# Kernel optimization log

Measured on AMD Instinct MI355X. Metric: run time of the kernel, lower is better.

## Reference

```python
import jax, jax.numpy as jnp
import numpy as np

N = 50000      # nodes
E = 800000     # edges
D = 128        # in_dim == hidden_dim
L = 5          # num GIN layers
G = 1000       # graphs in batch


def setup_inputs() -> dict:
    key = jax.random.key(0)
    ks = jax.random.split(key, 6)
    s = 1.0 / np.sqrt(D)  # keep activations stable over 5 layers
    x = jax.random.normal(ks[0], (N, D), dtype=jnp.float32)
    edge_index = jax.random.randint(ks[1], (2, E), 0, N, dtype=jnp.int32)
    batch = jnp.sort(jax.random.randint(ks[2], (N,), 0, G, dtype=jnp.int32))
    W1s = jax.random.normal(ks[3], (L, D, D), dtype=jnp.float32) * s
    b1s = jnp.zeros((L, D), jnp.float32)
    W2s = jax.random.normal(ks[4], (L, D, D), dtype=jnp.float32) * s
    b2s = jnp.zeros((L, D), jnp.float32)
    Wh = jax.random.normal(ks[5], (D, 1), dtype=jnp.float32) * s
    bh = jnp.zeros((1,), jnp.float32)
    return {"x": x, "edge_index": edge_index, "batch": batch,
            "W1s": W1s, "b1s": b1s, "W2s": W2s, "b2s": b2s,
            "Wh": Wh, "bh": bh}


def reference(x, edge_index, batch, W1s, b1s, W2s, b2s, Wh, bh):
    src, dst = edge_index[0], edge_index[1]
    h = x
    for l in range(L):
        # GINConv with eps=0: mlp(x + sum_{j->i} x_j)
        aggr = jax.ops.segment_sum(h[src], dst, num_segments=N)  # [N, D]
        z = h + aggr
        z = jax.nn.relu(z @ W1s[l] + b1s[l]) @ W2s[l] + b2s[l]   # 2-layer MLP
        h = jax.nn.relu(z)  # outer F.relu; dropout is identity in eval
    # global mean pool per graph
    sums = jax.ops.segment_sum(h, batch, num_segments=G)                     # [G, D]
    cnts = jax.ops.segment_sum(jnp.ones((N, 1), h.dtype), batch, num_segments=G)
    pooled = sums / jnp.maximum(cnts, 1.0)
    return pooled @ Wh + bh  # [G, 1] logits
```

## Files before the change

kernel.cpp:

```cpp
#include <hip/hip_runtime.h>
#include <hip/hip_bf16.h>

#define D 128
#define SLOTS 64
#define CSTR 72
#define BCAP 9216

typedef short short8 __attribute__((ext_vector_type(8)));
typedef float f32x4 __attribute__((ext_vector_type(4)));
typedef unsigned short u16;
typedef unsigned int u32;

static __device__ __forceinline__ u16 f2bf(float f) {
  union { float f; unsigned u; } v; v.f = f;
  unsigned r = v.u + 0x7FFF + ((v.u >> 16) & 1);
  return (u16)(r >> 16);
}
static __device__ __forceinline__ float bf2f(u16 h) {
  union { unsigned u; float f; } v; v.u = ((unsigned)h) << 16;
  return v.f;
}

__global__ __launch_bounds__(1024) void prep_kernel(
    const int* __restrict__ src, const int* __restrict__ dst,
    const float* __restrict__ x, const float* __restrict__ W1,
    const float* __restrict__ W2, int* __restrict__ gcount,
    u32* __restrict__ bedge, u16* __restrict__ W1th, u16* __restrict__ W1tl,
    u16* __restrict__ W2th, u16* __restrict__ W2tl, u32* __restrict__ xp,
    u32* __restrict__ hp, int E, int nbk, int wtotal, int nPairs,
    int nA, int nB, int nC, int N, int rowsP) {
  __shared__ int cnt[128];
  __shared__ int base[128];
  int b = blockIdx.x, t = threadIdx.x;
  if (b < nA) {
    if (t < nbk) cnt[t] = 0;
    __syncthreads();
    int e = b * 1024 + t;
    int bk = 0, p = 0;
    u32 payload = 0;
    bool valid = e < E;
    if (valid) {
      int d = dst[e];
      bk = d >> 9;
      payload = ((u32)src[e] << 9) | (u32)(d & 511);
      p = atomicAdd(&cnt[bk], 1);
    }
    __syncthreads();
    if (t < nbk) base[t] = cnt[t] ? atomicAdd(&gcount[t], cnt[t]) : 0;
    __syncthreads();
    if (valid) {
      int pos = base[bk] + p;
      if (pos < BCAP) bedge[(size_t)bk * BCAP + pos] = payload;
    }
  } else if (b < nA + nB) {
    int idx = (b - nA) * 1024 + t;
    if (idx < wtotal) {
      int l = idx >> 14;
      int r = idx & 16383;
      int j = r & 7;
      int lane = (r >> 3) & 63;
      int tt = r >> 9;
      int kt = tt >> 3, nt = tt & 7;
      int k = kt * 32 + (lane >> 4) * 8 + j;
      int n = nt * 16 + (lane & 15);
      size_t s = (size_t)l * D * D + (size_t)k * D + n;
      float w1 = W1[s], w2 = W2[s];
      u16 h1 = f2bf(w1), h2 = f2bf(w2);
      W1th[idx] = h1; W1tl[idx] = f2bf(w1 - bf2f(h1));
      W2th[idx] = h2; W2tl[idx] = f2bf(w2 - bf2f(h2));
    }
  } else if (b < nA + nB + nC) {
    int i0 = (b - nA - nB) * 4096 + t * 4;
    if (i0 < nPairs) {
      int node = i0 >> 6, pr = i0 & 63;
      float4 f0 = ((const float4*)x)[i0 >> 1];
      float4 f1 = ((const float4*)x)[(i0 >> 1) + 1];
      uint4 o;
      o.x = ((u32)f2bf(f0.y) << 16) | f2bf(f0.x);
      o.y = ((u32)f2bf(f0.w) << 16) | f2bf(f0.z);
      o.z = ((u32)f2bf(f1.y) << 16) | f2bf(f1.x);
      o.w = ((u32)f2bf(f1.w) << 16) | f2bf(f1.z);
      *(uint4*)(xp + ((size_t)(pr >> 5) * rowsP + node) * 32 + (pr & 31)) = o;
    }
  } else {
    if (t < 64) {
      xp[((size_t)(t >> 5) * rowsP + N) * 32 + (t & 31)] = 0;
      hp[((size_t)(t >> 5) * rowsP + N) * 32 + (t & 31)] = 0;
    }
  }
}

__global__ __launch_bounds__(1024) void binB_kernel(
    const int* __restrict__ gcount, const u32* __restrict__ bedge,
    int* __restrict__ deg, u16* __restrict__ colidx, int N) {
  __shared__ int cnt2[512];
  int b = blockIdx.x;
  int t = threadIdx.x;
  if (t < 512) cnt2[t] = 0;
  __syncthreads();
  int count = min(gcount[b], BCAP);
  const u32* lst = bedge + (size_t)b * BCAP;
  for (int i = t; i < count; i += 1024) {
    u32 v = lst[i];
    int local = v & 511;
    int slot = atomicAdd(&cnt2[local], 1);
    if (slot < SLOTS)
      colidx[((size_t)(b << 9) + local) * CSTR + slot] = (u16)(v >> 9);
  }
  __syncthreads();
  if (t < 512) {
    int node = (b << 9) + t;
    if (node < N) deg[node] = min(cnt2[t], SLOTS);
  }
  for (int i = t; i < 512 * CSTR; i += 1024) {
    int local = i / CSTR;
    int slot = i - local * CSTR;
    int node = (b << 9) + local;
    if (node < N && slot >= min(cnt2[local], SLOTS))
      colidx[((size_t)(b << 9) + local) * CSTR + slot] = (u16)N;
  }
}

__global__ __launch_bounds__(256) void aggregate_kernel(
    const u32* __restrict__ hp, const int* __restrict__ deg,
    const u16* __restrict__ colidx, u32* __restrict__ zp, int N, int rowsP) {
  int p = blockIdx.x & 1;
  int chunk = blockIdx.x >> 1;
  int lane = threadIdx.x & 63;
  int wave = threadIdx.x >> 6;
  int g = lane >> 3, c = lane & 7;
  int node = chunk * 32 + wave * 8 + g;
  bool live = node < N;
  const uint4* hpp = (const uint4*)(hp + (size_t)p * rowsP * 32);
  int e = live ? deg[node] : 0;
  int em = max(e, __shfl_xor(e, 8, 64));
  em = max(em, __shfl_xor(em, 16, 64));
  em = max(em, __shfl_xor(em, 32, 64));
  const u16* nbr = colidx + (size_t)(live ? node : 0) * CSTR;
  uint4 s = hpp[(size_t)(live ? node : N) * 8 + c];
  float a0 = bf2f((u16)(s.x & 0xffff)), a1 = bf2f((u16)(s.x >> 16));
  float a2 = bf2f((u16)(s.y & 0xffff)), a3 = bf2f((u16)(s.y >> 16));
  float a4 = bf2f((u16)(s.z & 0xffff)), a5 = bf2f((u16)(s.z >> 16));
  float a6 = bf2f((u16)(s.w & 0xffff)), a7 = bf2f((u16)(s.w >> 16));
  for (int k = 0; k < em; k += 8) {
    int idx[8];
    uint4 v[8];
#pragma unroll
    for (int i = 0; i < 8; ++i) idx[i] = nbr[k + i];
#pragma unroll
    for (int i = 0; i < 8; ++i) v[i] = hpp[(size_t)idx[i] * 8 + c];
#pragma unroll
    for (int i = 0; i < 8; ++i) {
      a0 += bf2f((u16)(v[i].x & 0xffff)); a1 += bf2f((u16)(v[i].x >> 16));
      a2 += bf2f((u16)(v[i].y & 0xffff)); a3 += bf2f((u16)(v[i].y >> 16));
      a4 += bf2f((u16)(v[i].z & 0xffff)); a5 += bf2f((u16)(v[i].z >> 16));
      a6 += bf2f((u16)(v[i].w & 0xffff)); a7 += bf2f((u16)(v[i].w >> 16));
    }
  }
  if (live) {
    uint4 o;
    o.x = ((u32)f2bf(a1) << 16) | f2bf(a0);
    o.y = ((u32)f2bf(a3) << 16) | f2bf(a2);
    o.z = ((u32)f2bf(a5) << 16) | f2bf(a4);
    o.w = ((u32)f2bf(a7) << 16) | f2bf(a6);
    ((uint4*)(zp + (size_t)p * rowsP * 32))[(size_t)node * 8 + c] = o;
  }
}

template <int STAGE>
__global__ __launch_bounds__(256) void gemm_kernel(
    const u16* __restrict__ A, const u16* __restrict__ Wth, const u16* __restrict__ Wtl,
    const float* __restrict__ bias, u16* __restrict__ outp,
    const float* __restrict__ Wh, const int* __restrict__ batch, float* __restrict__ gsum,
    int nrows, int rowsP) {
  __shared__ __attribute__((aligned(16))) u16 ldsW[32768];
  u16* ldsWh = ldsW;
  u16* ldsWl = ldsW + 16384;
  int tid = threadIdx.x;
  {
    const uint4* gh = (const uint4*)Wth;
    const uint4* gl = (const uint4*)Wtl;
    uint4 th[8], tl[8];
#pragma unroll
    for (int i = 0; i < 8; ++i) { th[i] = gh[tid + i * 256]; tl[i] = gl[tid + i * 256]; }
    uint4* lh = (uint4*)ldsWh;
    uint4* ll = (uint4*)ldsWl;
#pragma unroll
    for (int i = 0; i < 8; ++i) { lh[tid + i * 256] = th[i]; ll[tid + i * 256] = tl[i]; }
  }
  int wave = tid >> 6, lane = tid & 63;
  int quad = lane >> 4, l16 = lane & 15;
  int rowbase = blockIdx.x * 128 + wave * 32;
  int mc0 = min(rowbase + l16, nrows - 1);
  int mc1 = min(rowbase + 16 + l16, nrows - 1);

  short8 a0[4], a1[4];
#pragma unroll
  for (int kt = 0; kt < 4; ++kt) {
    if (STAGE == 0) {
      const u16* base = A + ((size_t)(kt >> 1) * rowsP) * 64 + (kt & 1) * 32 + quad * 8;
      a0[kt] = *(const short8*)(base + (size_t)mc0 * 64);
      a1[kt] = *(const short8*)(base + (size_t)mc1 * 64);
    } else {
      a0[kt] = *(const short8*)(A + (size_t)mc0 * D + kt * 32 + quad * 8);
      a1[kt] = *(const short8*)(A + (size_t)mc1 * D + kt * 32 + quad * 8);
    }
  }

  __syncthreads();

  f32x4 acc[2][8];
  f32x4 zero = {0.f, 0.f, 0.f, 0.f};
#pragma unroll
  for (int mt = 0; mt < 2; ++mt)
#pragma unroll
    for (int nt = 0; nt < 8; ++nt) acc[mt][nt] = zero;

#pragma unroll
  for (int kt = 0; kt < 4; ++kt) {
#pragma unroll
    for (int nt = 0; nt < 8; ++nt) {
      int fo = ((kt * 8 + nt) * 64 + lane) * 8;
      short8 bh = *(const short8*)(ldsWh + fo);
      short8 bl = *(const short8*)(ldsWl + fo);
      acc[0][nt] = __builtin_amdgcn_mfma_f32_16x16x32_bf16(a0[kt], bh, acc[0][nt], 0, 0, 0);
      acc[0][nt] = __builtin_amdgcn_mfma_f32_16x16x32_bf16(a0[kt], bl, acc[0][nt], 0, 0, 0);
      acc[1][nt] = __builtin_amdgcn_mfma_f32_16x16x32_bf16(a1[kt], bh, acc[1][nt], 0, 0, 0);
      acc[1][nt] = __builtin_amdgcn_mfma_f32_16x16x32_bf16(a1[kt], bl, acc[1][nt], 0, 0, 0);
    }
  }

  if (STAGE == 2) {
    float dotr[2][4] = {{0.f, 0.f, 0.f, 0.f}, {0.f, 0.f, 0.f, 0.f}};
#pragma unroll
    for (int nt = 0; nt < 8; ++nt) {
      int col = nt * 16 + l16;
      float bv = bias[col];
      float wv = Wh[col];
#pragma unroll
      for (int mt = 0; mt < 2; ++mt)
#pragma unroll
        for (int r = 0; r < 4; ++r)
          dotr[mt][r] += fmaxf(acc[mt][nt][r] + bv, 0.f) * wv;
    }
#pragma unroll
    for (int m = 1; m < 16; m <<= 1) {
#pragma unroll
      for (int mt = 0; mt < 2; ++mt)
#pragma unroll
        for (int r = 0; r < 4; ++r) dotr[mt][r] += __shfl_xor(dotr[mt][r], m, 64);
    }
    if (l16 == 0) {
#pragma unroll
      for (int mt = 0; mt < 2; ++mt)
#pragma unroll
        for (int r = 0; r < 4; ++r) {
          int row = rowbase + mt * 16 + quad * 4 + r;
          if (row < nrows) atomicAdd(&gsum[batch[row]], dotr[mt][r]);
        }
    }
  } else {
    __syncthreads();
#pragma unroll
    for (int nt = 0; nt < 8; ++nt) {
      float bv = bias[nt * 16 + l16];
#pragma unroll
      for (int mt = 0; mt < 2; ++mt)
#pragma unroll
        for (int r = 0; r < 4; ++r) {
          int lrow = wave * 32 + mt * 16 + quad * 4 + r;
          ldsW[lrow * 136 + nt * 16 + l16] = f2bf(fmaxf(acc[mt][nt][r] + bv, 0.f));
        }
    }
    __syncthreads();
#pragma unroll
    for (int i = 0; i < 8; ++i) {
      int chunk = i * 256 + tid;
      int r = chunk >> 4;
      int cc = (chunk & 15) * 8;
      int row = blockIdx.x * 128 + r;
      if (row < nrows) {
        uint4 v = *(const uint4*)(ldsW + r * 136 + cc);
        if (STAGE == 0) {
          *(uint4*)(outp + (size_t)row * D + cc) = v;
        } else {
          *(uint4*)(outp + ((size_t)(cc >> 6) * rowsP + row) * 64 + (cc & 63)) = v;
        }
      }
    }
  }
}

__global__ void pool_final_kernel(const float* __restrict__ gsum, const int* __restrict__ batch,
                                  const float* __restrict__ bh, float* __restrict__ out,
                                  int G, int N) {
  int g = blockIdx.x * 256 + threadIdx.x;
  if (g >= G) return;
  int lo = 0, hi = N;
  while (lo < hi) { int mid = (lo + hi) >> 1; if (batch[mid] < g) lo = mid + 1; else hi = mid; }
  int lo2 = lo, hi2 = N;
  while (lo2 < hi2) { int mid = (lo2 + hi2) >> 1; if (batch[mid] < g + 1) lo2 = mid + 1; else hi2 = mid; }
  int c = lo2 - lo;
  out[g] = gsum[g] / fmaxf((float)c, 1.f) + bh[0];
}

extern "C" void kernel_launch(void* const* d_in, const int* in_sizes, int n_in,
                              void* d_out, int out_size, void* d_ws, size_t ws_size,
                              hipStream_t stream) {
  const float* x   = (const float*)d_in[0];
  const int* eidx  = (const int*)d_in[1];
  const int* batch = (const int*)d_in[2];
  const float* W1s = (const float*)d_in[3];
  const float* b1s = (const float*)d_in[4];
  const float* W2s = (const float*)d_in[5];
  const float* b2s = (const float*)d_in[6];
  const float* Wh  = (const float*)d_in[7];
  const float* bh  = (const float*)d_in[8];
  float* out = (float*)d_out;

  int N = in_sizes[0] / D;
  int E = in_sizes[1] / 2;
  int G = out_size;
  int L = in_sizes[3] / (D * D);
  int nbk = (N + 511) >> 9;
  int wtotal = L * D * D;
  int nPairs = N * D / 2;
  int rowsP = N + 1;

  const int* src = eidx;
  const int* dst = eidx + E;

  char* p = (char*)d_ws;
  auto alloc = [&](size_t b) { char* r = p; p += (b + 255) & ~(size_t)255; return r; };
  u16*   hpnl   = (u16*)  alloc((size_t)2 * rowsP * 64 * 2);
  u16*   xpnl   = (u16*)  alloc((size_t)2 * rowsP * 64 * 2);
  u16*   zpnl   = (u16*)  alloc((size_t)2 * rowsP * 64 * 2);
  u16*   yb     = (u16*)  alloc((size_t)N * D * 2);
  size_t zbytes = (size_t)G * 4 + 512;
  char*  zblk   =         alloc(zbytes);
  float* gsum   = (float*)zblk;
  int*   gcount = (int*)(zblk + (size_t)G * 4);
  int*   deg    = (int*)  alloc((size_t)N * 4);
  u16*   colidx = (u16*)  alloc((size_t)N * CSTR * 2);
  u32*   bedge  = (u32*)  alloc((size_t)128 * BCAP * 4);
  u16*   W1th   = (u16*)  alloc((size_t)L * D * D * 2);
  u16*   W1tl   = (u16*)  alloc((size_t)L * D * D * 2);
  u16*   W2th   = (u16*)  alloc((size_t)L * D * D * 2);
  u16*   W2tl   = (u16*)  alloc((size_t)L * D * D * 2);

  hipMemsetAsync(zblk, 0, zbytes, stream);

  int nA = (E + 1023) / 1024;
  int nB = (wtotal + 1023) / 1024;
  int nC = (nPairs / 4 + 1023) / 1024;
  prep_kernel<<<nA + nB + nC + 1, 1024, 0, stream>>>(
      src, dst, x, W1s, W2s, gcount, bedge, W1th, W1tl, W2th, W2tl,
      (u32*)xpnl, (u32*)hpnl, E, nbk, wtotal, nPairs, nA, nB, nC, N, rowsP);
  binB_kernel<<<nbk, 1024, 0, stream>>>(gcount, bedge, deg, colidx, N);

  int agg_blocks = 2 * ((N + 31) / 32);
  int gemm_blocks = (N + 127) / 128;
  for (int l = 0; l < L; ++l) {
    const u16* hin = (l == 0) ? xpnl : hpnl;
    size_t wo = (size_t)l * D * D;
    aggregate_kernel<<<agg_blocks, 256, 0, stream>>>(
        (const u32*)hin, deg, colidx, (u32*)zpnl, N, rowsP);
    gemm_kernel<0><<<gemm_blocks, 256, 0, stream>>>(
        zpnl, W1th + wo, W1tl + wo, b1s + (size_t)l * D, yb,
        nullptr, nullptr, nullptr, N, rowsP);
    if (l < L - 1) {
      gemm_kernel<1><<<gemm_blocks, 256, 0, stream>>>(
          yb, W2th + wo, W2tl + wo, b2s + (size_t)l * D, hpnl,
          nullptr, nullptr, nullptr, N, rowsP);
    } else {
      gemm_kernel<2><<<gemm_blocks, 256, 0, stream>>>(
          yb, W2th + wo, W2tl + wo, b2s + (size_t)l * D, nullptr,
          Wh, batch, gsum, N, rowsP);
    }
  }
  pool_final_kernel<<<(G + 255) / 256, 256, 0, stream>>>(gsum, batch, bh, out, G, N);
}
```

Baseline: 391.0 us.

## Fuse the two MLP GEMMs into one kernel keeping hidden activations in LDS

Merges the first and second MLP GEMM kernels into one per-layer mlp_kernel. The intermediate relu(zW1+b1) tile is written to shared memory and reloaded as MFMA A-fragments instead of round-tripping through a global bf16 buffer. Both weight matrices are prefetched into registers up front, with W2 swapped into LDS between the two GEMMs. This removes one launch per layer and the global write and read of the hidden tensor, at the cost of higher register pressure (four 8-element uint4 weight arrays held at once) and extra block barriers.

```diff
diff --git a/kernel.cpp b/kernel.cpp
--- a/kernel.cpp
+++ b/kernel.cpp
@@ -167,44 +167,48 @@
   }
 }
 
-template <int STAGE>
-__global__ __launch_bounds__(256) void gemm_kernel(
-    const u16* __restrict__ A, const u16* __restrict__ Wth, const u16* __restrict__ Wtl,
-    const float* __restrict__ bias, u16* __restrict__ outp,
-    const float* __restrict__ Wh, const int* __restrict__ batch, float* __restrict__ gsum,
+template <int LAST>
+__global__ __launch_bounds__(256) void mlp_kernel(
+    const u16* __restrict__ A,
+    const u16* __restrict__ W1th, const u16* __restrict__ W1tl, const float* __restrict__ b1,
+    const u16* __restrict__ W2th, const u16* __restrict__ W2tl, const float* __restrict__ b2,
+    u16* __restrict__ hout, const float* __restrict__ Wh,
+    const int* __restrict__ batch, float* __restrict__ gsum,
     int nrows, int rowsP) {
   __shared__ __attribute__((aligned(16))) u16 ldsW[32768];
   u16* ldsWh = ldsW;
   u16* ldsWl = ldsW + 16384;
   int tid = threadIdx.x;
-  {
-    const uint4* gh = (const uint4*)Wth;
-    const uint4* gl = (const uint4*)Wtl;
-    uint4 th[8], tl[8];
-#pragma unroll
-    for (int i = 0; i < 8; ++i) { th[i] = gh[tid + i * 256]; tl[i] = gl[tid + i * 256]; }
-    uint4* lh = (uint4*)ldsWh;
-    uint4* ll = (uint4*)ldsWl;
-#pragma unroll
-    for (int i = 0; i < 8; ++i) { lh[tid + i * 256] = th[i]; ll[tid + i * 256] = tl[i]; }
-  }
   int wave = tid >> 6, lane = tid & 63;
   int quad = lane >> 4, l16 = lane & 15;
   int rowbase = blockIdx.x * 128 + wave * 32;
   int mc0 = min(rowbase + l16, nrows - 1);
   int mc1 = min(rowbase + 16 + l16, nrows - 1);
 
+  uint4 t1h[8], t1l[8], t2h[8], t2l[8];
+  {
+    const uint4* g1h = (const uint4*)W1th;
+    const uint4* g1l = (const uint4*)W1tl;
+    const uint4* g2h = (const uint4*)W2th;
+    const uint4* g2l = (const uint4*)W2tl;
+#pragma unroll
+    for (int i = 0; i < 8; ++i) {
+      t1h[i] = g1h[tid + i * 256]; t1l[i] = g1l[tid + i * 256];
+      t2h[i] = g2h[tid + i * 256]; t2l[i] = g2l[tid + i * 256];
+    }
+  }
   short8 a0[4], a1[4];
 #pragma unroll
   for (int kt = 0; kt < 4; ++kt) {
-    if (STAGE == 0) {
-      const u16* base = A + ((size_t)(kt >> 1) * rowsP) * 64 + (kt & 1) * 32 + quad * 8;
-      a0[kt] = *(const short8*)(base + (size_t)mc0 * 64);
-      a1[kt] = *(const short8*)(base + (size_t)mc1 * 64);
-    } else {
-      a0[kt] = *(const short8*)(A + (size_t)mc0 * D + kt * 32 + quad * 8);
-      a1[kt] = *(const short8*)(A + (size_t)mc1 * D + kt * 32 + quad * 8);
-    }
+    const u16* base = A + ((size_t)(kt >> 1) * rowsP) * 64 + (kt & 1) * 32 + quad * 8;
+    a0[kt] = *(const short8*)(base + (size_t)mc0 * 64);
+    a1[kt] = *(const short8*)(base + (size_t)mc1 * 64);
+  }
+  {
+    uint4* lh = (uint4*)ldsWh;
+    uint4* ll = (uint4*)ldsWl;
+#pragma unroll
+    for (int i = 0; i < 8; ++i) { lh[tid + i * 256] = t1h[i]; ll[tid + i * 256] = t1l[i]; }
   }
 
   __syncthreads();
@@ -215,7 +219,6 @@
   for (int mt = 0; mt < 2; ++mt)
 #pragma unroll
     for (int nt = 0; nt < 8; ++nt) acc[mt][nt] = zero;
-
 #pragma unroll
   for (int kt = 0; kt < 4; ++kt) {
 #pragma unroll
@@ -230,12 +233,62 @@
     }
   }
 
-  if (STAGE == 2) {
+  __syncthreads();
+
+  u16* yw = ldsW + wave * 32 * 136;
+#pragma unroll
+  for (int nt = 0; nt < 8; ++nt) {
+    float bv = b1[nt * 16 + l16];
+#pragma unroll
+    for (int mt = 0; mt < 2; ++mt)
+#pragma unroll
+      for (int r = 0; r < 4; ++r) {
+        int lrow = mt * 16 + quad * 4 + r;
+        yw[lrow * 136 + nt * 16 + l16] = f2bf(fmaxf(acc[mt][nt][r] + bv, 0.f));
+      }
+  }
+  short8 p0[4], p1[4];
+#pragma unroll
+  for (int kt = 0; kt < 4; ++kt) {
+    p0[kt] = *(const short8*)(yw + (size_t)l16 * 136 + kt * 32 + quad * 8);
+    p1[kt] = *(const short8*)(yw + (size_t)(16 + l16) * 136 + kt * 32 + quad * 8);
+  }
+
+  __syncthreads();
+
+  {
+    uint4* lh = (uint4*)ldsWh;
+    uint4* ll = (uint4*)ldsWl;
+#pragma unroll
+    for (int i = 0; i < 8; ++i) { lh[tid + i * 256] = t2h[i]; ll[tid + i * 256] = t2l[i]; }
+  }
+
+  __syncthreads();
+
+#pragma unroll
+  for (int mt = 0; mt < 2; ++mt)
+#pragma unroll
+    for (int nt = 0; nt < 8; ++nt) acc[mt][nt] = zero;
+#pragma unroll
+  for (int kt = 0; kt < 4; ++kt) {
+#pragma unroll
+    for (int nt = 0; nt < 8; ++nt) {
+      int fo = ((kt * 8 + nt) * 64 + lane) * 8;
+      short8 bh = *(const short8*)(ldsWh + fo);
+      short8 bl = *(const short8*)(ldsWl + fo);
+      acc[0][nt] = __builtin_amdgcn_mfma_f32_16x16x32_bf16(p0[kt], bh, acc[0][nt], 0, 0, 0);
+      acc[0][nt] = __builtin_amdgcn_mfma_f32_16x16x32_bf16(p0[kt], bl, acc[0][nt], 0, 0, 0);
+      acc[1][nt] = __builtin_amdgcn_mfma_f32_16x16x32_bf16(p1[kt], bh, acc[1][nt], 0, 0, 0);
+      acc[1][nt] = __builtin_amdgcn_mfma_f32_16x16x32_bf16(p1[kt], bl, acc[1][nt], 0, 0, 0);
+    }
+  }
+
+  if (LAST) {
     float dotr[2][4] = {{0.f, 0.f, 0.f, 0.f}, {0.f, 0.f, 0.f, 0.f}};
 #pragma unroll
     for (int nt = 0; nt < 8; ++nt) {
       int col = nt * 16 + l16;
-      float bv = bias[col];
+      float bv = b2[col];
       float wv = Wh[col];
 #pragma unroll
       for (int mt = 0; mt < 2; ++mt)
@@ -263,7 +316,7 @@
     __syncthreads();
 #pragma unroll
     for (int nt = 0; nt < 8; ++nt) {
-      float bv = bias[nt * 16 + l16];
+      float bv = b2[nt * 16 + l16];
 #pragma unroll
       for (int mt = 0; mt < 2; ++mt)
 #pragma unroll
@@ -281,11 +334,7 @@
       int row = blockIdx.x * 128 + r;
       if (row < nrows) {
         uint4 v = *(const uint4*)(ldsW + r * 136 + cc);
-        if (STAGE == 0) {
-          *(uint4*)(outp + (size_t)row * D + cc) = v;
-        } else {
-          *(uint4*)(outp + ((size_t)(cc >> 6) * rowsP + row) * 64 + (cc & 63)) = v;
-        }
+        *(uint4*)(hout + ((size_t)(cc >> 6) * rowsP + row) * 64 + (cc & 63)) = v;
       }
     }
   }
@@ -335,7 +384,6 @@
   u16*   hpnl   = (u16*)  alloc((size_t)2 * rowsP * 64 * 2);
   u16*   xpnl   = (u16*)  alloc((size_t)2 * rowsP * 64 * 2);
   u16*   zpnl   = (u16*)  alloc((size_t)2 * rowsP * 64 * 2);
-  u16*   yb     = (u16*)  alloc((size_t)N * D * 2);
   size_t zbytes = (size_t)G * 4 + 512;
   char*  zblk   =         alloc(zbytes);
   float* gsum   = (float*)zblk;
@@ -359,23 +407,22 @@
   binB_kernel<<<nbk, 1024, 0, stream>>>(gcount, bedge, deg, colidx, N);
 
   int agg_blocks = 2 * ((N + 31) / 32);
-  int gemm_blocks = (N + 127) / 128;
+  int mlp_blocks = (N + 127) / 128;
   for (int l = 0; l < L; ++l) {
     const u16* hin = (l == 0) ? xpnl : hpnl;
     size_t wo = (size_t)l * D * D;
     aggregate_kernel<<<agg_blocks, 256, 0, stream>>>(
         (const u32*)hin, deg, colidx, (u32*)zpnl, N, rowsP);
-    gemm_kernel<0><<<gemm_blocks, 256, 0, stream>>>(
-        zpnl, W1th + wo, W1tl + wo, b1s + (size_t)l * D, yb,
-        nullptr, nullptr, nullptr, N, rowsP);
     if (l < L - 1) {
-      gemm_kernel<1><<<gemm_blocks, 256, 0, stream>>>(
-          yb, W2th + wo, W2tl + wo, b2s + (size_t)l * D, hpnl,
-          nullptr, nullptr, nullptr, N, rowsP);
+      mlp_kernel<0><<<mlp_blocks, 256, 0, stream>>>(
+          zpnl, W1th + wo, W1tl + wo, b1s + (size_t)l * D,
+          W2th + wo, W2tl + wo, b2s + (size_t)l * D,
+          hpnl, nullptr, nullptr, nullptr, N, rowsP);
     } else {
-      gemm_kernel<2><<<gemm_blocks, 256, 0, stream>>>(
-          yb, W2th + wo, W2tl + wo, b2s + (size_t)l * D, nullptr,
-          Wh, batch, gsum, N, rowsP);
+      mlp_kernel<1><<<mlp_blocks, 256, 0, stream>>>(
+          zpnl, W1th + wo, W1tl + wo, b1s + (size_t)l * D,
+          W2th + wo, W2tl + wo, b2s + (size_t)l * D,
+          nullptr, Wh, batch, gsum, N, rowsP);
     }
   }
   pool_final_kernel<<<(G + 255) / 256, 256, 0, stream>>>(gsum, batch, bh, out, G, N);
```

After: 380.5 us. 2.7% less time.
